# Performance work log

Hardware: AMD Instinct MI355X
Metric: run time of the kernel (lower is better)

Reference implementation:

```python
import jax, jax.numpy as jnp
import numpy as np

B, N, D, H = 4, 2048, 256, 4
HD = D // H


def _linear(x, W, b):
    return x @ W.T + b


def _rotate_half(x):
    # pairs (x0,x1) -> (-x1, x0)
    x1 = x[..., ::2]
    x2 = x[..., 1::2]
    return jnp.stack((-x2, x1), axis=-1).reshape(x.shape)


def _layernorm(x, g, b, eps=1e-5):
    m = jnp.mean(x, axis=-1, keepdims=True)
    v = jnp.mean((x - m) ** 2, axis=-1, keepdims=True)
    return (x - m) / jnp.sqrt(v + eps) * g + b


def _ffn(x, W1, b1, g, be, W2, b2):
    h = _linear(x, W1, b1)
    h = _layernorm(h, g, be)
    h = jax.nn.gelu(h, approximate=False)
    return _linear(h, W2, b2)


def _self_block(x, enc, Wqkv, bqkv, Wout, bout, W1, b1, g, be, W2, b2):
    Bq, Nq, _ = x.shape
    qkv = _linear(x, Wqkv, bqkv).reshape(Bq, Nq, H, HD, 3).transpose(0, 2, 1, 3, 4)  # [B,H,N,HD,3]
    q, k, v = qkv[..., 0], qkv[..., 1], qkv[..., 2]
    q = q * enc[0] + _rotate_half(q) * enc[1]
    k = k * enc[0] + _rotate_half(k) * enc[1]
    scale = HD ** -0.5
    sim = jnp.einsum('bhid,bhjd->bhij', q, k) * scale
    attn = jax.nn.softmax(sim, axis=-1)
    ctx = jnp.einsum('bhij,bhjd->bhid', attn, v)
    msg = _linear(ctx.transpose(0, 2, 1, 3).reshape(Bq, Nq, D), Wout, bout)
    return x + _ffn(jnp.concatenate([x, msg], axis=-1), W1, b1, g, be, W2, b2)


def _cross_block(x0, x1, Wqk, bqk, Wv, bv, Wo, bo, W1, b1, g, be, W2, b2):
    def heads(t):
        return t.reshape(t.shape[0], t.shape[1], H, HD).transpose(0, 2, 1, 3)  # [B,H,N,HD]
    qk0 = heads(_linear(x0, Wqk, bqk))
    qk1 = heads(_linear(x1, Wqk, bqk))
    v0 = heads(_linear(x0, Wv, bv))
    v1 = heads(_linear(x1, Wv, bv))
    s = (HD ** -0.5) ** 0.5
    qk0 = qk0 * s
    qk1 = qk1 * s
    sim = jnp.einsum('bhid,bhjd->bhij', qk0, qk1)
    attn01 = jax.nn.softmax(sim, axis=-1)   # over j (x1 tokens)
    attn10 = jax.nn.softmax(sim, axis=-2)   # over i (x0 tokens)
    m0 = jnp.einsum('bhij,bhjd->bhid', attn01, v1)
    m1 = jnp.einsum('bhij,bhid->bhjd', attn10, v0)
    def unheads(t):
        return t.transpose(0, 2, 1, 3).reshape(t.shape[0], t.shape[2], D)
    m0 = _linear(unheads(m0), Wo, bo)
    m1 = _linear(unheads(m1), Wo, bo)
    x0 = x0 + _ffn(jnp.concatenate([x0, m0], axis=-1), W1, b1, g, be, W2, b2)
    x1 = x1 + _ffn(jnp.concatenate([x1, m1], axis=-1), W1, b1, g, be, W2, b2)
    return x0, x1


def setup_inputs() -> dict:
    key = jax.random.key(0)
    ks = jax.random.split(key, 32)
    std = 0.05

    def rn(k, shape, s=std):
        return jax.random.normal(k, shape, dtype=jnp.float32) * s

    def enc(k):
        ang = jax.random.uniform(k, (B, 1, N, HD // 2), dtype=jnp.float32) * (2 * np.pi)
        cos = jnp.repeat(jnp.cos(ang), 2, axis=-1)
        sin = jnp.repeat(jnp.sin(ang), 2, axis=-1)
        return jnp.stack([cos, sin], axis=0)  # [2,B,1,N,HD]

    return {
        'desc0': rn(ks[0], (B, N, D), 1.0),
        'desc1': rn(ks[1], (B, N, D), 1.0),
        'enc0': enc(ks[2]),
        'enc1': enc(ks[3]),
        's_Wqkv': rn(ks[4], (3 * D, D)), 's_bqkv': jnp.zeros((3 * D,), jnp.float32),
        's_Wout': rn(ks[5], (D, D)), 's_bout': jnp.zeros((D,), jnp.float32),
        's_W1': rn(ks[6], (2 * D, 2 * D)), 's_b1': jnp.zeros((2 * D,), jnp.float32),
        's_g': jnp.ones((2 * D,), jnp.float32), 's_be': jnp.zeros((2 * D,), jnp.float32),
        's_W2': rn(ks[7], (D, 2 * D)), 's_b2': jnp.zeros((D,), jnp.float32),
        'c_Wqk': rn(ks[8], (D, D)), 'c_bqk': jnp.zeros((D,), jnp.float32),
        'c_Wv': rn(ks[9], (D, D)), 'c_bv': jnp.zeros((D,), jnp.float32),
        'c_Wo': rn(ks[10], (D, D)), 'c_bo': jnp.zeros((D,), jnp.float32),
        'c_W1': rn(ks[11], (2 * D, 2 * D)), 'c_b1': jnp.zeros((2 * D,), jnp.float32),
        'c_g': jnp.ones((2 * D,), jnp.float32), 'c_be': jnp.zeros((2 * D,), jnp.float32),
        'c_W2': rn(ks[12], (D, 2 * D)), 'c_b2': jnp.zeros((D,), jnp.float32),
    }


def reference(desc0, desc1, enc0, enc1,
              s_Wqkv, s_bqkv, s_Wout, s_bout, s_W1, s_b1, s_g, s_be, s_W2, s_b2,
              c_Wqk, c_bqk, c_Wv, c_bv, c_Wo, c_bo, c_W1, c_b1, c_g, c_be, c_W2, c_b2):
    d0 = _self_block(desc0, enc0, s_Wqkv, s_bqkv, s_Wout, s_bout, s_W1, s_b1, s_g, s_be, s_W2, s_b2)
    d1 = _self_block(desc1, enc1, s_Wqkv, s_bqkv, s_Wout, s_bout, s_W1, s_b1, s_g, s_be, s_W2, s_b2)
    return _cross_block(d0, d1, c_Wqk, c_bqk, c_Wv, c_bv, c_Wo, c_bo, c_W1, c_b1, c_g, c_be, c_W2, c_b2)
```

## Files before the change

### kernel.cpp

```cpp
#include <hip/hip_runtime.h>
#include <cstddef>

#define NTOK 2048
#define BDIM 4
#define DIM 256
#define NHEAD 4
#define MROWS 8192
#define M2 16384
#define NMu ((size_t)MROWS * DIM)

typedef unsigned short u16;
typedef __attribute__((ext_vector_type(8))) short short8;
typedef __attribute__((ext_vector_type(4))) float f32x4;

#if __has_builtin(__builtin_amdgcn_exp2f)
#define EXP2(x) __builtin_amdgcn_exp2f(x)
#else
#define EXP2(x) exp2f(x)
#endif

__device__ __forceinline__ u16 f2bf(float x) {
  union { float f; unsigned u; } c; c.f = x;
  unsigned r = c.u + 0x7FFFu + ((c.u >> 16) & 1u);
  return (u16)(r >> 16);
}
__device__ __forceinline__ float bf2f(u16 u) {
  union { unsigned u; float f; } c; c.u = ((unsigned)u) << 16;
  return c.f;
}

__device__ __forceinline__ void glds16(const void* g, void* l) {
  __builtin_amdgcn_global_load_lds(
      (const __attribute__((address_space(1))) unsigned int*)g,
      (__attribute__((address_space(3))) unsigned int*)l, 16, 0, 0);
}

__global__ __launch_bounds__(256) void gemm_bf16_kernel(
    const u16* __restrict__ A, int lda,
    const u16* __restrict__ A2, int lda2, int kSplit,
    const u16* __restrict__ W,
    const float* __restrict__ bias0, const float* __restrict__ bias1,
    int nsplit, float os0, float os1,
    u16* __restrict__ Yb0, int ldy0,
    u16* __restrict__ Yb1, int ldy1,
    int K)
{
  __shared__ u16 As[2 * 4096];
  __shared__ u16 Bs[2 * 4096];
  const int t = threadIdx.x;
  const int m0 = blockIdx.y * 128, n0 = blockIdx.x * 128;
  const int r4 = t >> 2, c8 = (t & 3) * 8;
  const int lane = t & 63, w = t >> 6;
  const int cl = lane & 15, quad = lane >> 4;
  const int wm = (w >> 1) * 64, wn = (w & 1) * 64;

  f32x4 acc[4][4];
#pragma unroll
  for (int i = 0; i < 4; ++i)
#pragma unroll
    for (int j = 0; j < 4; ++j) acc[i][j] = (f32x4){0.f, 0.f, 0.f, 0.f};

  for (int k0 = 0; k0 < K; k0 += 64) {
    const u16* Ab; int la; int kk;
    if (k0 < kSplit) { Ab = A; la = lda; kk = k0; }
    else             { Ab = A2; la = lda2; kk = k0 - kSplit; }
    const u16* ag = Ab + (size_t)(m0 + r4) * la + kk + c8;
    const u16* bg = W + (size_t)(n0 + r4) * K + k0 + c8;
    __syncthreads();
#pragma unroll
    for (int kh = 0; kh < 2; ++kh) {
      glds16(ag + kh * 32, &As[kh * 4096 + t * 8]);
      glds16(ag + (size_t)64 * la + kh * 32, &As[kh * 4096 + 2048 + t * 8]);
      glds16(bg + kh * 32, &Bs[kh * 4096 + t * 8]);
      glds16(bg + (size_t)64 * K + kh * 32, &Bs[kh * 4096 + 2048 + t * 8]);
    }
    __syncthreads();

#pragma unroll
    for (int kh = 0; kh < 2; ++kh) {
      short8 af[4], bfr[4];
#pragma unroll
      for (int i = 0; i < 4; ++i)
        af[i] = *(const short8*)&As[kh * 4096 + (wm + i * 16 + cl) * 32 + quad * 8];
#pragma unroll
      for (int i = 0; i < 4; ++i)
        bfr[i] = *(const short8*)&Bs[kh * 4096 + (wn + i * 16 + cl) * 32 + quad * 8];
#pragma unroll
      for (int mt = 0; mt < 4; ++mt)
#pragma unroll
        for (int nt = 0; nt < 4; ++nt)
          acc[mt][nt] = __builtin_amdgcn_mfma_f32_16x16x32_bf16(
              af[mt], bfr[nt], acc[mt][nt], 0, 0, 0);
    }
  }

#pragma unroll
  for (int mt = 0; mt < 4; ++mt)
#pragma unroll
    for (int nt = 0; nt < 4; ++nt) {
      const int colg = n0 + wn + nt * 16 + cl;
      const bool first = colg < nsplit;
      const int c2 = first ? colg : colg - nsplit;
      const float bs = first ? bias0[c2] : bias1[c2];
      const float os = first ? os0 : os1;
      u16* yb = first ? Yb0 : Yb1;
      const int ly = first ? ldy0 : ldy1;
#pragma unroll
      for (int r = 0; r < 4; ++r) {
        const int rowg = m0 + wm + mt * 16 + quad * 4 + r;
        yb[(size_t)rowg * ly + c2] = f2bf((acc[mt][nt][r] + bs) * os);
      }
    }
}

__global__ __launch_bounds__(256) void gemm64_kernel(
    const u16* __restrict__ A, int lda,
    const u16* __restrict__ W,
    const float* __restrict__ bias,
    const u16* __restrict__ resb, int ldrb,
    float* __restrict__ Yf, int ldyf,
    u16* __restrict__ Yb, int ldyb,
    int K)
{
  __shared__ u16 As[2 * 2048];
  __shared__ u16 Bs[2 * 2048];
  const int t = threadIdx.x;
  const int m0 = blockIdx.y * 64, n0 = blockIdx.x * 64;
  const int r8 = t >> 2, c8 = (t & 3) * 8;
  const int lane = t & 63, w = t >> 6;
  const int cl = lane & 15, quad = lane >> 4;
  const int wm = (w >> 1) * 32, wn = (w & 1) * 32;

  f32x4 acc[2][2];
#pragma unroll
  for (int i = 0; i < 2; ++i)
#pragma unroll
    for (int j = 0; j < 2; ++j) acc[i][j] = (f32x4){0.f, 0.f, 0.f, 0.f};

  for (int k0 = 0; k0 < K; k0 += 64) {
    const u16* ag = A + (size_t)(m0 + r8) * lda + k0 + c8;
    const u16* bg = W + (size_t)(n0 + r8) * K + k0 + c8;
    __syncthreads();
#pragma unroll
    for (int kh = 0; kh < 2; ++kh) {
      glds16(ag + kh * 32, &As[kh * 2048 + t * 8]);
      glds16(bg + kh * 32, &Bs[kh * 2048 + t * 8]);
    }
    __syncthreads();

#pragma unroll
    for (int kh = 0; kh < 2; ++kh) {
      short8 af[2], bfr[2];
#pragma unroll
      for (int i = 0; i < 2; ++i)
        af[i] = *(const short8*)&As[kh * 2048 + (wm + i * 16 + cl) * 32 + quad * 8];
#pragma unroll
      for (int j = 0; j < 2; ++j)
        bfr[j] = *(const short8*)&Bs[kh * 2048 + (wn + j * 16 + cl) * 32 + quad * 8];
#pragma unroll
      for (int mt = 0; mt < 2; ++mt)
#pragma unroll
        for (int nt = 0; nt < 2; ++nt)
          acc[mt][nt] = __builtin_amdgcn_mfma_f32_16x16x32_bf16(
              af[mt], bfr[nt], acc[mt][nt], 0, 0, 0);
    }
  }

#pragma unroll
  for (int mt = 0; mt < 2; ++mt)
#pragma unroll
    for (int nt = 0; nt < 2; ++nt) {
      const int colg = n0 + wn + nt * 16 + cl;
      const float bs = bias[colg];
#pragma unroll
      for (int r = 0; r < 4; ++r) {
        const int rowg = m0 + wm + mt * 16 + quad * 4 + r;
        float v = acc[mt][nt][r] + bs;
        if (resb) v += bf2f(resb[(size_t)rowg * ldrb + colg]);
        if (Yf) Yf[(size_t)rowg * ldyf + colg] = v;
        if (Yb) Yb[(size_t)rowg * ldyb + colg] = f2bf(v);
      }
    }
}

__global__ __launch_bounds__(256) void pack_wfuse_kernel(
    const float* w0, const float* w1, const float* w2, const float* w3,
    const float* w4, const float* d0, const float* d1,
    u16* __restrict__ wb, u16* __restrict__ descb,
    const float* __restrict__ W1, const float* __restrict__ Wo,
    const float* __restrict__ b1, const float* __restrict__ bo,
    const float* __restrict__ cW1, const float* __restrict__ cWo,
    const float* __restrict__ cb1, const float* __restrict__ cbo,
    u16* __restrict__ W1f, u16* __restrict__ cW1f,
    float* __restrict__ b1f, float* __restrict__ cb1f)
{
  __shared__ float rowh[256];
  const int bid = blockIdx.x;
  const int t = threadIdx.x;
  if (bid < 4672) {
    const size_t idx4 = ((size_t)bid * 256 + t) * 4;
    const float* src; u16* dst; size_t off;
    if (idx4 < 589824) {
      off = idx4; dst = wb + idx4;
      if      (idx4 < 196608) { src = w0; }
      else if (idx4 < 327680) { src = w1; off -= 196608; }
      else if (idx4 < 393216) { src = w2; off -= 327680; }
      else if (idx4 < 458752) { src = w3; off -= 393216; }
      else                    { src = w4; off -= 458752; }
    } else {
      size_t o = idx4 - 589824;
      dst = descb + o;
      if (o < NMu) { src = d0; off = o; }
      else         { src = d1; off = o - NMu; }
    }
    float4 v = *(const float4*)(src + off);
    ushort4 ov;
    ov.x = f2bf(v.x); ov.y = f2bf(v.y); ov.z = f2bf(v.z); ov.w = f2bf(v.w);
    *(ushort4*)dst = ov;
  } else {
    const int idx = bid - 4672;
    const int n = idx & 511, sel = idx >> 9;
    const float* Ws = sel ? cW1 : W1;
    const float* Wos = sel ? cWo : Wo;
    u16* out = sel ? cW1f : W1f;
    rowh[t] = Ws[(size_t)n * 512 + 256 + t];
    out[(size_t)n * 512 + t] = f2bf(Ws[(size_t)n * 512 + t]);
    __syncthreads();
    float acc = 0.f;
    for (int m = 0; m < 256; ++m) acc += rowh[m] * Wos[(size_t)m * 256 + t];
    out[(size_t)n * 512 + 256 + t] = f2bf(acc);
    if (t == 0) {
      const float* bos = sel ? cbo : bo;
      const float* b1s = sel ? cb1 : b1;
      float a = b1s[n];
      for (int m = 0; m < 256; ++m) a += rowh[m] * bos[m];
      (sel ? cb1f : b1f)[n] = a;
    }
  }
}

__global__ __launch_bounds__(256) void rope_tv_kernel(
    const u16* __restrict__ qkv, const float* __restrict__ enc0,
    const float* __restrict__ enc1,
    u16* __restrict__ Q, u16* __restrict__ K, u16* __restrict__ Vt)
{
  __shared__ u16 Vl[64 * 264];
  const int blk = blockIdx.x;
  const int t = threadIdx.x;
  const int hf = blk >> 7;
  const float* enc = hf ? enc1 : enc0;
  const float QSC = 0.18033688011112042f;

  for (int p = 0; p < 32; ++p) {
    const int j = p * 256 + t;
    const int i = j & 31;
    const int h = (j >> 5) & 3;
    const int lt = j >> 7;
    const int m = blk * 64 + lt;
    const int lm = m & (MROWS - 1);
    const u16* src = qkv + (size_t)m * 768 + h * 192 + i * 6;
    const unsigned a0 = *(const unsigned*)(src);
    const unsigned a1 = *(const unsigned*)(src + 2);
    const unsigned a2 = *(const unsigned*)(src + 4);
    const float q0 = bf2f((u16)a0), k0 = bf2f((u16)(a0 >> 16));
    const float v0 = bf2f((u16)a1), q1 = bf2f((u16)(a1 >> 16));
    const float k1 = bf2f((u16)a2), v1 = bf2f((u16)(a2 >> 16));
    const float c = enc[(size_t)lm * 64 + 2 * i];
    const float s = enc[(size_t)MROWS * 64 + (size_t)lm * 64 + 2 * i];
    const size_t o = (size_t)m * 256 + h * 64 + 2 * i;
    *(unsigned*)(Q + o) = (unsigned)f2bf((q0 * c - q1 * s) * QSC) |
                          ((unsigned)f2bf((q1 * c + q0 * s) * QSC) << 16);
    *(unsigned*)(K + o) = (unsigned)f2bf(k0 * c - k1 * s) |
                          ((unsigned)f2bf(k1 * c + k0 * s) << 16);
    *(unsigned*)&Vl[lt * 264 + h * 64 + 2 * i] =
        (unsigned)f2bf(v0) | ((unsigned)f2bf(v1) << 16);
  }
  __syncthreads();

  const int bz = blk >> 5, n0 = (blk & 31) * 64;
  const int dd = t >> 2, qr = t & 3;
#pragma unroll
  for (int h = 0; h < 4; ++h) {
    union { u16 u[16]; uint4 v[2]; } pk;
#pragma unroll
    for (int jj = 0; jj < 16; ++jj)
      pk.u[jj] = Vl[(qr * 16 + jj) * 264 + h * 64 + dd];
    u16* dst = Vt + ((size_t)((bz * NHEAD + h) * 64 + dd)) * NTOK + n0 + qr * 16;
    *(uint4*)dst = pk.v[0];
    *(uint4*)(dst + 8) = pk.v[1];
  }
}

__global__ __launch_bounds__(256) void transpose_v_kernel(
    const u16* __restrict__ in, u16* __restrict__ out)
{
  __shared__ u16 Tl[64][72];
  const int bz = blockIdx.z, h = blockIdx.y;
  const int n0 = blockIdx.x * 64;
  const int t = threadIdx.x;
  {
    const int row = t >> 2, c16 = (t & 3) * 16;
    const u16* src = in + (size_t)(bz * NTOK + n0 + row) * 256 + h * 64 + c16;
    *(uint4*)&Tl[row][c16] = *(const uint4*)src;
    *(uint4*)&Tl[row][c16 + 8] = *(const uint4*)(src + 8);
  }
  __syncthreads();
  const int d = t >> 2, qr = t & 3;
  union { u16 u[16]; uint4 v[2]; } pk;
#pragma unroll
  for (int j = 0; j < 16; ++j) pk.u[j] = Tl[qr * 16 + j][d];
  u16* dst = out + ((size_t)((bz * NHEAD + h) * 64 + d)) * NTOK + n0 + qr * 16;
  *(uint4*)dst = pk.v[0];
  *(uint4*)(dst + 8) = pk.v[1];
}

__global__ __launch_bounds__(256, 2) void attn5_kernel(
    const u16* __restrict__ Qb, const u16* __restrict__ Kb,
    const u16* __restrict__ Vtb, u16* __restrict__ Ou, int cross)
{
  __shared__ u16 Ks[2][64 * 64];
  __shared__ u16 Vs[2][64 * 64];
  __shared__ u16 Ps[4][32 * 64];

  const int hw = blockIdx.x;
  const int li = hw >> 3;
  const int y  = (hw & 7) * 4 + (li >> 4);
  const int n0 = (li & 15) * 128;

  const int h2 = y >> 4, b = (y >> 2) & 3, h = y & 3;
  const int kh = cross ? (1 - h2) : h2;
  const int qrowbase = (h2 * 4 + b) * NTOK;
  const int krowbase = (kh * 4 + b) * NTOK;
  const int vz = kh * 4 + b;
  const int t = threadIdx.x, lane = t & 63, w = t >> 6;
  const int cl = lane & 15, quad = lane >> 4;
  const int q0 = w * 32;
  const int fsw = (cl & 7) << 4;

  short8 bq[2][2];
#pragma unroll
  for (int c = 0; c < 2; ++c) {
    const u16* qsrc = Qb + (size_t)(qrowbase + n0 + q0 + c * 16 + cl) * 256 +
                      h * 64 + quad * 8;
    bq[c][0] = *(const short8*)qsrc;
    bq[c][1] = *(const short8*)(qsrc + 32);
  }

  float l_r[2] = {0.f, 0.f};
  f32x4 o[2][4];
#pragma unroll
  for (int c = 0; c < 2; ++c)
#pragma unroll
    for (int i = 0; i < 4; ++i) o[c][i] = (f32x4){0.f, 0.f, 0.f, 0.f};

  const int srow = t >> 2;
  const int scb = (t & 3) * 32;
  const int ssw = (srow & 7) << 4;
  const u16* Kg = Kb + (size_t)(krowbase + srow) * 256 + h * 64 + (t & 3) * 16;
  const u16* Vg = Vtb + ((size_t)(vz * NHEAD + h) * 64 + srow) * NTOK + (t & 3) * 16;

  uint4 ka0 = *(const uint4*)Kg, ka1 = *(const uint4*)(Kg + 8);
  uint4 va0 = *(const uint4*)Vg, va1 = *(const uint4*)(Vg + 8);
  {
    char* kd = (char*)&Ks[0][srow * 64];
    *(uint4*)(kd + (scb ^ ssw)) = ka0;
    *(uint4*)(kd + ((scb + 16) ^ ssw)) = ka1;
    char* vd = (char*)&Vs[0][srow * 64];
    *(uint4*)(vd + (scb ^ ssw)) = va0;
    *(uint4*)(vd + ((scb + 16) ^ ssw)) = va1;
  }
  Kg += 64 * 256; Vg += 64;
  ka0 = *(const uint4*)Kg; ka1 = *(const uint4*)(Kg + 8);
  va0 = *(const uint4*)Vg; va1 = *(const uint4*)(Vg + 8);
  __syncthreads();

  for (int tile = 0; tile < 32; ++tile) {
    const int cur = tile & 1, nxt = cur ^ 1;

    f32x4 sf[2][4];
    __builtin_amdgcn_s_setprio(1);
#pragma unroll
    for (int kb = 0; kb < 4; ++kb) {
      const char* kr = (const char*)&Ks[cur][(kb * 16 + cl) * 64];
      short8 ak0 = *(const short8*)(kr + ((quad * 16) ^ fsw));
      short8 ak1 = *(const short8*)(kr + ((quad * 16 + 64) ^ fsw));
#pragma unroll
      for (int c = 0; c < 2; ++c) {
        f32x4 acc = (f32x4){0.f, 0.f, 0.f, 0.f};
        acc = __builtin_amdgcn_mfma_f32_16x16x32_bf16(ak0, bq[c][0], acc, 0, 0, 0);
        acc = __builtin_amdgcn_mfma_f32_16x16x32_bf16(ak1, bq[c][1], acc, 0, 0, 0);
        sf[c][kb] = acc;
      }
    }
    __builtin_amdgcn_s_setprio(0);

    if (tile < 31) {
      char* kd = (char*)&Ks[nxt][srow * 64];
      *(uint4*)(kd + (scb ^ ssw)) = ka0;
      *(uint4*)(kd + ((scb + 16) ^ ssw)) = ka1;
      if (tile < 30) {
        Kg += 64 * 256;
        ka0 = *(const uint4*)Kg; ka1 = *(const uint4*)(Kg + 8);
      }
    }

#pragma unroll
    for (int c = 0; c < 2; ++c) {
      float rs = 0.f;
#pragma unroll
      for (int kb = 0; kb < 4; ++kb)
#pragma unroll
        for (int r = 0; r < 4; ++r) {
          const float p = EXP2(sf[c][kb][r]);
          sf[c][kb][r] = p; rs += p;
        }
      rs += __shfl_xor(rs, 16);
      rs += __shfl_xor(rs, 32);
      l_r[c] += rs;
      char* pd = (char*)&Ps[w][(c * 16 + cl) * 64];
#pragma unroll
      for (int kb = 0; kb < 4; ++kb) {
        unsigned d0 = __builtin_amdgcn_perm(__float_as_uint(sf[c][kb][1]),
                                            __float_as_uint(sf[c][kb][0]), 0x07060302u);
        unsigned d1 = __builtin_amdgcn_perm(__float_as_uint(sf[c][kb][3]),
                                            __float_as_uint(sf[c][kb][2]), 0x07060302u);
        uint2 pk; pk.x = d0; pk.y = d1;
        *(uint2*)(pd + ((kb * 32 + quad * 8) ^ fsw)) = pk;
      }
    }

    short8 bp[2][2];
#pragma unroll
    for (int c = 0; c < 2; ++c) {
      const char* pr = (const char*)&Ps[w][(c * 16 + cl) * 64];
      bp[c][0] = *(const short8*)(pr + ((quad * 16) ^ fsw));
      bp[c][1] = *(const short8*)(pr + ((quad * 16 + 64) ^ fsw));
    }
    __builtin_amdgcn_s_setprio(1);
#pragma unroll
    for (int db = 0; db < 4; ++db) {
      const char* vr = (const char*)&Vs[cur][(db * 16 + cl) * 64];
      short8 av0 = *(const short8*)(vr + ((quad * 16) ^ fsw));
      short8 av1 = *(const short8*)(vr + ((quad * 16 + 64) ^ fsw));
#pragma unroll
      for (int c = 0; c < 2; ++c) {
        o[c][db] = __builtin_amdgcn_mfma_f32_16x16x32_bf16(av0, bp[c][0], o[c][db], 0, 0, 0);
        o[c][db] = __builtin_amdgcn_mfma_f32_16x16x32_bf16(av1, bp[c][1], o[c][db], 0, 0, 0);
      }
    }
    __builtin_amdgcn_s_setprio(0);

    if (tile < 31) {
      char* vd = (char*)&Vs[nxt][srow * 64];
      *(uint4*)(vd + (scb ^ ssw)) = va0;
      *(uint4*)(vd + ((scb + 16) ^ ssw)) = va1;
      if (tile < 30) {
        Vg += 64;
        va0 = *(const uint4*)Vg; va1 = *(const uint4*)(Vg + 8);
      }
    }
    __syncthreads();
  }

#pragma unroll
  for (int c = 0; c < 2; ++c) {
    const float inv = 1.f / l_r[c];
    const size_t rowo = (size_t)(qrowbase + n0 + q0 + c * 16 + cl) * 256 + h * 64;
#pragma unroll
    for (int db = 0; db < 4; ++db) {
      ushort4 st;
      st.x = f2bf(o[c][db][0] * inv); st.y = f2bf(o[c][db][1] * inv);
      st.z = f2bf(o[c][db][2] * inv); st.w = f2bf(o[c][db][3] * inv);
      *(ushort4*)(Ou + rowo + db * 16 + quad * 4) = st;
    }
  }
}

__global__ __launch_bounds__(256) void ln_gelu_kernel(
    const u16* __restrict__ Hm, const float* __restrict__ g,
    const float* __restrict__ be, u16* __restrict__ out)
{
  const int rowi = blockIdx.x * 4 + (threadIdx.x >> 6);
  const int lane = threadIdx.x & 63;
  const u16* row = Hm + (size_t)rowi * 512 + lane * 8;
  u16* orow = out + (size_t)rowi * 512 + lane * 8;
  uint4 raw = *(const uint4*)row;
  float x[8];
  const unsigned* rw = (const unsigned*)&raw;
#pragma unroll
  for (int i = 0; i < 4; ++i) {
    x[2 * i]     = bf2f((u16)rw[i]);
    x[2 * i + 1] = bf2f((u16)(rw[i] >> 16));
  }
  float s = 0.f;
#pragma unroll
  for (int i = 0; i < 8; ++i) s += x[i];
#pragma unroll
  for (int off = 32; off; off >>= 1) s += __shfl_xor(s, off);
  const float mean = s * (1.f / 512.f);
  float s2 = 0.f;
#pragma unroll
  for (int i = 0; i < 8; ++i) { const float d = x[i] - mean; s2 += d * d; }
#pragma unroll
  for (int off = 32; off; off >>= 1) s2 += __shfl_xor(s2, off);
  const float rstd = rsqrtf(s2 * (1.f / 512.f) + 1e-5f);
  unsigned ov[4];
#pragma unroll
  for (int i = 0; i < 4; ++i) {
    const int c = lane * 8 + 2 * i;
    const float y0 = (x[2 * i] - mean) * rstd * g[c] + be[c];
    const float y1 = (x[2 * i + 1] - mean) * rstd * g[c + 1] + be[c + 1];
    const float g0 = 0.5f * y0 * (1.f + erff(y0 * 0.70710678118654752f));
    const float g1 = 0.5f * y1 * (1.f + erff(y1 * 0.70710678118654752f));
    ov[i] = (unsigned)f2bf(g0) | ((unsigned)f2bf(g1) << 16);
  }
  *(uint4*)orow = *(uint4*)ov;
}

extern "C" void kernel_launch(void* const* d_in, const int* in_sizes, int n_in,
                              void* d_out, int out_size, void* d_ws, size_t ws_size,
                              hipStream_t stream) {
  const float* desc0  = (const float*)d_in[0];
  const float* desc1  = (const float*)d_in[1];
  const float* enc0   = (const float*)d_in[2];
  const float* enc1   = (const float*)d_in[3];
  const float* s_Wqkv = (const float*)d_in[4];
  const float* s_bqkv = (const float*)d_in[5];
  const float* s_Wout = (const float*)d_in[6];
  const float* s_bout = (const float*)d_in[7];
  const float* s_W1   = (const float*)d_in[8];
  const float* s_b1   = (const float*)d_in[9];
  const float* s_g    = (const float*)d_in[10];
  const float* s_be   = (const float*)d_in[11];
  const float* s_W2   = (const float*)d_in[12];
  const float* s_b2   = (const float*)d_in[13];
  const float* c_Wqk  = (const float*)d_in[14];
  const float* c_bqk  = (const float*)d_in[15];
  const float* c_Wv   = (const float*)d_in[16];
  const float* c_bv   = (const float*)d_in[17];
  const float* c_Wo   = (const float*)d_in[18];
  const float* c_bo   = (const float*)d_in[19];
  const float* c_W1   = (const float*)d_in[20];
  const float* c_b1   = (const float*)d_in[21];
  const float* c_g    = (const float*)d_in[22];
  const float* c_be   = (const float*)d_in[23];
  const float* c_W2   = (const float*)d_in[24];
  const float* c_b2   = (const float*)d_in[25];

  u16* U = (u16*)d_ws;
  u16* descb = U + 0 * NMu;
  u16* qkvb  = U + 2 * NMu;
  u16* ctxb  = U + 2 * NMu;
  u16* Qu    = U + 8 * NMu;
  u16* Ku    = U + 10 * NMu;
  u16* Vt    = U + 14 * NMu;
  u16* hbufb = U + 12 * NMu;
  u16* hb2   = U + 16 * NMu;
  float* b1f = (float*)(U + 20 * NMu);
  float* cb1f = b1f + 512;
  u16* s_b   = U + 21 * NMu;
  u16* wb    = U + 23 * NMu;

  u16* Wqkvb = wb;
  u16* W2b   = wb + 196608;
  u16* cQKVb = wb + 327680;
  u16* cW2b  = wb + 458752;
  u16* W1f   = wb + 589824;
  u16* cW1f  = wb + 851968;

  float* outf = (float*)d_out;

  const dim3 tv_grid(NTOK / 64, NHEAD, 8);
  const int lng_blocks  = M2 / 4;
  const float csc = 0.42466090014400953f;

  hipLaunchKernelGGL(pack_wfuse_kernel, dim3(5696), dim3(256), 0, stream,
                     s_Wqkv, s_W2, c_Wqk, c_Wv, c_W2, desc0, desc1, wb, descb,
                     s_W1, s_Wout, s_b1, s_bout, c_W1, c_Wo, c_b1, c_bo,
                     W1f, cW1f, b1f, cb1f);

  hipLaunchKernelGGL(gemm_bf16_kernel, dim3(6, 128), dim3(256), 0, stream,
                     descb, 256, (const u16*)nullptr, 0, 1 << 30, Wqkvb,
                     s_bqkv, (const float*)nullptr, 1 << 30, 1.f, 1.f,
                     qkvb, 768, (u16*)nullptr, 0, 256);
  hipLaunchKernelGGL(rope_tv_kernel, dim3(256), dim3(256), 0, stream,
                     qkvb, enc0, enc1, Qu, Ku, Vt);
  hipLaunchKernelGGL(attn5_kernel, dim3(512), dim3(256), 0, stream,
                     Qu, Ku, Vt, ctxb, 0);
  hipLaunchKernelGGL(gemm_bf16_kernel, dim3(4, 128), dim3(256), 0, stream,
                     descb, 256, ctxb, 256, 256, W1f,
                     b1f, (const float*)nullptr, 1 << 30, 1.f, 1.f,
                     hbufb, 512, (u16*)nullptr, 0, 512);
  hipLaunchKernelGGL(ln_gelu_kernel, dim3(lng_blocks), dim3(256), 0, stream,
                     hbufb, s_g, s_be, hb2);
  hipLaunchKernelGGL(gemm64_kernel, dim3(4, 256), dim3(256), 0, stream,
                     hb2, 512, W2b, s_b2, descb, 256,
                     (float*)nullptr, 0, s_b, 256, 512);

  u16* qkb = Qu;
  u16* vb  = Ku;
  hipLaunchKernelGGL(gemm_bf16_kernel, dim3(4, 128), dim3(256), 0, stream,
                     s_b, 256, (const u16*)nullptr, 0, 1 << 30, cQKVb,
                     c_bqk, c_bv, 256, csc, 1.f,
                     qkb, 256, vb, 256, 256);
  hipLaunchKernelGGL(transpose_v_kernel, tv_grid, dim3(256), 0, stream, vb, Vt);
  hipLaunchKernelGGL(attn5_kernel, dim3(512), dim3(256), 0, stream,
                     qkb, qkb, Vt, ctxb, 1);
  hipLaunchKernelGGL(gemm_bf16_kernel, dim3(4, 128), dim3(256), 0, stream,
                     s_b, 256, ctxb, 256, 256, cW1f,
                     cb1f, (const float*)nullptr, 1 << 30, 1.f, 1.f,
                     hbufb, 512, (u16*)nullptr, 0, 512);
  hipLaunchKernelGGL(ln_gelu_kernel, dim3(lng_blocks), dim3(256), 0, stream,
                     hbufb, c_g, c_be, hb2);
  hipLaunchKernelGGL(gemm64_kernel, dim3(4, 256), dim3(256), 0, stream,
                     hb2, 512, cW2b, c_b2, s_b, 256,
                     outf, 256, (u16*)nullptr, 0, 512);
}
```

Baseline: 377.2 us.

## Switch attention to 32x32x16 MFMA and pass P through registers instead of LDS

Rewrites the attention kernel to use 32x32x16 bf16 MFMA tiles in place of 16x16x32 tiles. The QK^T accumulator layout now lines up with the PV operand layout, so the exp'd probabilities are packed with v_cvt_pk_bf16_f32. Half-wave lane swaps then form the A operand, which removes the per-warp LDS write/read of P and its shared buffer. The aim is fewer LDS round trips and fewer MFMA issues per tile. In exchange, the epilogue now writes scalar bf16 stores and shuffles the row sums, which is less coalesced.

```diff
diff --git a/kernel.cpp b/kernel.cpp
--- a/kernel.cpp
+++ b/kernel.cpp
@@ -12,6 +12,7 @@
 typedef unsigned short u16;
 typedef __attribute__((ext_vector_type(8))) short short8;
 typedef __attribute__((ext_vector_type(4))) float f32x4;
+typedef __attribute__((ext_vector_type(16))) float f32x16;
 
 #if __has_builtin(__builtin_amdgcn_exp2f)
 #define EXP2(x) __builtin_amdgcn_exp2f(x)
@@ -27,6 +28,11 @@
 __device__ __forceinline__ float bf2f(u16 u) {
   union { unsigned u; float f; } c; c.u = ((unsigned)u) << 16;
   return c.f;
+}
+__device__ __forceinline__ unsigned cvtpk(float lo, float hi) {
+  unsigned r;
+  asm("v_cvt_pk_bf16_f32 %0, %1, %2" : "=v"(r) : "v"(lo), "v"(hi));
+  return r;
 }
 
 __device__ __forceinline__ void glds16(const void* g, void* l) {
@@ -314,13 +320,12 @@
   *(uint4*)(dst + 8) = pk.v[1];
 }
 
-__global__ __launch_bounds__(256, 2) void attn5_kernel(
+__global__ __launch_bounds__(256, 2) void attn9_kernel(
     const u16* __restrict__ Qb, const u16* __restrict__ Kb,
     const u16* __restrict__ Vtb, u16* __restrict__ Ou, int cross)
 {
   __shared__ u16 Ks[2][64 * 64];
   __shared__ u16 Vs[2][64 * 64];
-  __shared__ u16 Ps[4][32 * 64];
 
   const int hw = blockIdx.x;
   const int li = hw >> 3;
@@ -333,25 +338,22 @@
   const int krowbase = (kh * 4 + b) * NTOK;
   const int vz = kh * 4 + b;
   const int t = threadIdx.x, lane = t & 63, w = t >> 6;
-  const int cl = lane & 15, quad = lane >> 4;
+  const int l31 = lane & 31, hi = lane >> 5;
   const int q0 = w * 32;
-  const int fsw = (cl & 7) << 4;
-
-  short8 bq[2][2];
-#pragma unroll
-  for (int c = 0; c < 2; ++c) {
-    const u16* qsrc = Qb + (size_t)(qrowbase + n0 + q0 + c * 16 + cl) * 256 +
-                      h * 64 + quad * 8;
-    bq[c][0] = *(const short8*)qsrc;
-    bq[c][1] = *(const short8*)(qsrc + 32);
-  }
-
-  float l_r[2] = {0.f, 0.f};
-  f32x4 o[2][4];
-#pragma unroll
-  for (int c = 0; c < 2; ++c)
-#pragma unroll
-    for (int i = 0; i < 4; ++i) o[c][i] = (f32x4){0.f, 0.f, 0.f, 0.f};
+  const int fsw = (l31 & 7) << 4;
+
+  short8 bq[4];
+  {
+    const u16* qsrc = Qb + (size_t)(qrowbase + n0 + q0 + l31) * 256 +
+                      h * 64 + hi * 8;
+#pragma unroll
+    for (int ks = 0; ks < 4; ++ks) bq[ks] = *(const short8*)(qsrc + ks * 16);
+  }
+
+  float l_r = 0.f;
+  f32x16 o0, o1;
+#pragma unroll
+  for (int i = 0; i < 16; ++i) { o0[i] = 0.f; o1[i] = 0.f; }
 
   const int srow = t >> 2;
   const int scb = (t & 3) * 32;
@@ -377,20 +379,17 @@
   for (int tile = 0; tile < 32; ++tile) {
     const int cur = tile & 1, nxt = cur ^ 1;
 
-    f32x4 sf[2][4];
+    f32x16 s0, s1;
+#pragma unroll
+    for (int i = 0; i < 16; ++i) { s0[i] = 0.f; s1[i] = 0.f; }
     __builtin_amdgcn_s_setprio(1);
 #pragma unroll
-    for (int kb = 0; kb < 4; ++kb) {
-      const char* kr = (const char*)&Ks[cur][(kb * 16 + cl) * 64];
-      short8 ak0 = *(const short8*)(kr + ((quad * 16) ^ fsw));
-      short8 ak1 = *(const short8*)(kr + ((quad * 16 + 64) ^ fsw));
-#pragma unroll
-      for (int c = 0; c < 2; ++c) {
-        f32x4 acc = (f32x4){0.f, 0.f, 0.f, 0.f};
-        acc = __builtin_amdgcn_mfma_f32_16x16x32_bf16(ak0, bq[c][0], acc, 0, 0, 0);
-        acc = __builtin_amdgcn_mfma_f32_16x16x32_bf16(ak1, bq[c][1], acc, 0, 0, 0);
-        sf[c][kb] = acc;
-      }
+    for (int ks = 0; ks < 4; ++ks) {
+      const int ofs = (ks * 32 + hi * 16) ^ fsw;
+      short8 ak0 = *(const short8*)((const char*)&Ks[cur][l31 * 64] + ofs);
+      short8 ak1 = *(const short8*)((const char*)&Ks[cur][(32 + l31) * 64] + ofs);
+      s0 = __builtin_amdgcn_mfma_f32_32x32x16_bf16(ak0, bq[ks], s0, 0, 0, 0);
+      s1 = __builtin_amdgcn_mfma_f32_32x32x16_bf16(ak1, bq[ks], s1, 0, 0, 0);
     }
     __builtin_amdgcn_s_setprio(0);
 
@@ -404,51 +403,42 @@
       }
     }
 
-#pragma unroll
-    for (int c = 0; c < 2; ++c) {
-      float rs = 0.f;
-#pragma unroll
-      for (int kb = 0; kb < 4; ++kb)
-#pragma unroll
-        for (int r = 0; r < 4; ++r) {
-          const float p = EXP2(sf[c][kb][r]);
-          sf[c][kb][r] = p; rs += p;
-        }
-      rs += __shfl_xor(rs, 16);
-      rs += __shfl_xor(rs, 32);
-      l_r[c] += rs;
-      char* pd = (char*)&Ps[w][(c * 16 + cl) * 64];
-#pragma unroll
-      for (int kb = 0; kb < 4; ++kb) {
-        unsigned d0 = __builtin_amdgcn_perm(__float_as_uint(sf[c][kb][1]),
-                                            __float_as_uint(sf[c][kb][0]), 0x07060302u);
-        unsigned d1 = __builtin_amdgcn_perm(__float_as_uint(sf[c][kb][3]),
-                                            __float_as_uint(sf[c][kb][2]), 0x07060302u);
-        uint2 pk; pk.x = d0; pk.y = d1;
-        *(uint2*)(pd + ((kb * 32 + quad * 8) ^ fsw)) = pk;
+    float rs = 0.f;
+#pragma unroll
+    for (int kg = 0; kg < 2; ++kg) {
+      float p[16];
+#pragma unroll
+      for (int r = 0; r < 16; ++r) {
+        p[r] = EXP2(kg ? s1[r] : s0[r]);
+        rs += p[r];
       }
-    }
-
-    short8 bp[2][2];
-#pragma unroll
-    for (int c = 0; c < 2; ++c) {
-      const char* pr = (const char*)&Ps[w][(c * 16 + cl) * 64];
-      bp[c][0] = *(const short8*)(pr + ((quad * 16) ^ fsw));
-      bp[c][1] = *(const short8*)(pr + ((quad * 16 + 64) ^ fsw));
-    }
-    __builtin_amdgcn_s_setprio(1);
-#pragma unroll
-    for (int db = 0; db < 4; ++db) {
-      const char* vr = (const char*)&Vs[cur][(db * 16 + cl) * 64];
-      short8 av0 = *(const short8*)(vr + ((quad * 16) ^ fsw));
-      short8 av1 = *(const short8*)(vr + ((quad * 16 + 64) ^ fsw));
-#pragma unroll
-      for (int c = 0; c < 2; ++c) {
-        o[c][db] = __builtin_amdgcn_mfma_f32_16x16x32_bf16(av0, bp[c][0], o[c][db], 0, 0, 0);
-        o[c][db] = __builtin_amdgcn_mfma_f32_16x16x32_bf16(av1, bp[c][1], o[c][db], 0, 0, 0);
+      unsigned pa4[4], pb4[4], xa4[4], xb4[4];
+#pragma unroll
+      for (int g = 0; g < 4; ++g) {
+        pa4[g] = cvtpk(p[4 * g], p[4 * g + 1]);
+        pb4[g] = cvtpk(p[4 * g + 2], p[4 * g + 3]);
+        xa4[g] = (unsigned)__shfl_xor((int)pa4[g], 32);
+        xb4[g] = (unsigned)__shfl_xor((int)pb4[g], 32);
       }
-    }
-    __builtin_amdgcn_s_setprio(0);
+      __builtin_amdgcn_s_setprio(1);
+#pragma unroll
+      for (int k2 = 0; k2 < 2; ++k2) {
+        const int g0 = (2 * k2) & 3, g1 = (2 * k2 + 1) & 3;
+        union { unsigned u[4]; short8 s; } pa;
+        pa.u[0] = hi ? xa4[g1] : pa4[g0];
+        pa.u[1] = hi ? xb4[g1] : pb4[g0];
+        pa.u[2] = hi ? pa4[g1] : xa4[g0];
+        pa.u[3] = hi ? pb4[g1] : xb4[g0];
+        const int ks = kg * 2 + k2;
+        const int ofs = (ks * 32 + hi * 16) ^ fsw;
+        short8 bv0 = *(const short8*)((const char*)&Vs[cur][l31 * 64] + ofs);
+        short8 bv1 = *(const short8*)((const char*)&Vs[cur][(32 + l31) * 64] + ofs);
+        o0 = __builtin_amdgcn_mfma_f32_32x32x16_bf16(pa.s, bv0, o0, 0, 0, 0);
+        o1 = __builtin_amdgcn_mfma_f32_32x32x16_bf16(pa.s, bv1, o1, 0, 0, 0);
+      }
+      __builtin_amdgcn_s_setprio(0);
+    }
+    l_r += rs + __shfl_xor(rs, 32);
 
     if (tile < 31) {
       char* vd = (char*)&Vs[nxt][srow * 64];
@@ -463,16 +453,13 @@
   }
 
 #pragma unroll
-  for (int c = 0; c < 2; ++c) {
-    const float inv = 1.f / l_r[c];
-    const size_t rowo = (size_t)(qrowbase + n0 + q0 + c * 16 + cl) * 256 + h * 64;
-#pragma unroll
-    for (int db = 0; db < 4; ++db) {
-      ushort4 st;
-      st.x = f2bf(o[c][db][0] * inv); st.y = f2bf(o[c][db][1] * inv);
-      st.z = f2bf(o[c][db][2] * inv); st.w = f2bf(o[c][db][3] * inv);
-      *(ushort4*)(Ou + rowo + db * 16 + quad * 4) = st;
-    }
+  for (int r = 0; r < 16; ++r) {
+    const int qrow = (r & 3) + 8 * (r >> 2) + 4 * hi;
+    const float lq = __shfl(l_r, qrow);
+    const float inv = 1.f / lq;
+    const size_t rowo = (size_t)(qrowbase + n0 + q0 + qrow) * 256 + h * 64;
+    Ou[rowo + l31]      = f2bf(o0[r] * inv);
+    Ou[rowo + 32 + l31] = f2bf(o1[r] * inv);
   }
 }
 
@@ -585,7 +572,7 @@
                      qkvb, 768, (u16*)nullptr, 0, 256);
   hipLaunchKernelGGL(rope_tv_kernel, dim3(256), dim3(256), 0, stream,
                      qkvb, enc0, enc1, Qu, Ku, Vt);
-  hipLaunchKernelGGL(attn5_kernel, dim3(512), dim3(256), 0, stream,
+  hipLaunchKernelGGL(attn9_kernel, dim3(512), dim3(256), 0, stream,
                      Qu, Ku, Vt, ctxb, 0);
   hipLaunchKernelGGL(gemm_bf16_kernel, dim3(4, 128), dim3(256), 0, stream,
                      descb, 256, ctxb, 256, 256, W1f,
@@ -604,7 +591,7 @@
                      c_bqk, c_bv, 256, csc, 1.f,
                      qkb, 256, vb, 256, 256);
   hipLaunchKernelGGL(transpose_v_kernel, tv_grid, dim3(256), 0, stream, vb, Vt);
-  hipLaunchKernelGGL(attn5_kernel, dim3(512), dim3(256), 0, stream,
+  hipLaunchKernelGGL(attn9_kernel, dim3(512), dim3(256), 0, stream,
                      qkb, qkb, Vt, ctxb, 1);
   hipLaunchKernelGGL(gemm_bf16_kernel, dim3(4, 128), dim3(256), 0, stream,
                      s_b, 256, ctxb, 256, 256, cW1f,
```

Result: no change. 384.6 us (+2.0%).

## Prefetch next GEMM K-tile into registers while computing current tile

Applied to the files above, without the earlier changes.

Both bf16 GEMM kernels drop direct global-to-LDS loads and instead stage the next K tile in registers. Those loads are issued before the MFMA work on the current tile and written to LDS after it. The aim is to hide global memory latency behind compute without needing a second LDS buffer. The cost is extra VGPRs for the staging registers, possible occupancy loss, and explicit LDS writes replacing the async LDS loads.

```diff
diff --git a/kernel.cpp b/kernel.cpp
--- a/kernel.cpp
+++ b/kernel.cpp
@@ -29,11 +29,34 @@
   return c.f;
 }
 
-__device__ __forceinline__ void glds16(const void* g, void* l) {
-  __builtin_amdgcn_global_load_lds(
-      (const __attribute__((address_space(1))) unsigned int*)g,
-      (__attribute__((address_space(3))) unsigned int*)l, 16, 0, 0);
-}
+#define GB_GLOAD(k0)                                                       \
+  {                                                                        \
+    const u16* Ab; int la; int kk;                                         \
+    if ((k0) < kSplit) { Ab = A;  la = lda;  kk = (k0); }                  \
+    else               { Ab = A2; la = lda2; kk = (k0) - kSplit; }         \
+    const u16* ag = Ab + (size_t)(m0 + r4) * la + kk + c8;                 \
+    const u16* bg = W + (size_t)(n0 + r4) * K + (k0) + c8;                 \
+    ra[0] = *(const uint4*)(ag);                                           \
+    ra[1] = *(const uint4*)(ag + (size_t)64 * la);                         \
+    ra[2] = *(const uint4*)(ag + 32);                                      \
+    ra[3] = *(const uint4*)(ag + (size_t)64 * la + 32);                    \
+    rb[0] = *(const uint4*)(bg);                                           \
+    rb[1] = *(const uint4*)(bg + (size_t)64 * K);                          \
+    rb[2] = *(const uint4*)(bg + 32);                                      \
+    rb[3] = *(const uint4*)(bg + (size_t)64 * K + 32);                     \
+  }
+
+#define GB_LWRITE()                                                        \
+  {                                                                        \
+    *(uint4*)&As[t * 8]               = ra[0];                             \
+    *(uint4*)&As[2048 + t * 8]        = ra[1];                             \
+    *(uint4*)&As[4096 + t * 8]        = ra[2];                             \
+    *(uint4*)&As[4096 + 2048 + t * 8] = ra[3];                             \
+    *(uint4*)&Bs[t * 8]               = rb[0];                             \
+    *(uint4*)&Bs[2048 + t * 8]        = rb[1];                             \
+    *(uint4*)&Bs[4096 + t * 8]        = rb[2];                             \
+    *(uint4*)&Bs[4096 + 2048 + t * 8] = rb[3];                             \
+  }
 
 __global__ __launch_bounds__(256) void gemm_bf16_kernel(
     const u16* __restrict__ A, int lda,
@@ -60,21 +83,14 @@
 #pragma unroll
     for (int j = 0; j < 4; ++j) acc[i][j] = (f32x4){0.f, 0.f, 0.f, 0.f};
 
+  uint4 ra[4], rb[4];
+  GB_GLOAD(0);
+  GB_LWRITE();
+  __syncthreads();
+
   for (int k0 = 0; k0 < K; k0 += 64) {
-    const u16* Ab; int la; int kk;
-    if (k0 < kSplit) { Ab = A; la = lda; kk = k0; }
-    else             { Ab = A2; la = lda2; kk = k0 - kSplit; }
-    const u16* ag = Ab + (size_t)(m0 + r4) * la + kk + c8;
-    const u16* bg = W + (size_t)(n0 + r4) * K + k0 + c8;
-    __syncthreads();
-#pragma unroll
-    for (int kh = 0; kh < 2; ++kh) {
-      glds16(ag + kh * 32, &As[kh * 4096 + t * 8]);
-      glds16(ag + (size_t)64 * la + kh * 32, &As[kh * 4096 + 2048 + t * 8]);
-      glds16(bg + kh * 32, &Bs[kh * 4096 + t * 8]);
-      glds16(bg + (size_t)64 * K + kh * 32, &Bs[kh * 4096 + 2048 + t * 8]);
-    }
-    __syncthreads();
+    const bool more = (k0 + 64 < K);
+    if (more) GB_GLOAD(k0 + 64);
 
 #pragma unroll
     for (int kh = 0; kh < 2; ++kh) {
@@ -91,6 +107,12 @@
         for (int nt = 0; nt < 4; ++nt)
           acc[mt][nt] = __builtin_amdgcn_mfma_f32_16x16x32_bf16(
               af[mt], bfr[nt], acc[mt][nt], 0, 0, 0);
+    }
+
+    if (more) {
+      __syncthreads();
+      GB_LWRITE();
+      __syncthreads();
     }
   }
 
@@ -137,16 +159,31 @@
 #pragma unroll
     for (int j = 0; j < 2; ++j) acc[i][j] = (f32x4){0.f, 0.f, 0.f, 0.f};
 
+  uint4 ra[2], rb[2];
+#define G64_GLOAD(k0)                                                      \
+  {                                                                        \
+    const u16* ag = A + (size_t)(m0 + r8) * lda + (k0) + c8;               \
+    const u16* bg = W + (size_t)(n0 + r8) * K + (k0) + c8;                 \
+    ra[0] = *(const uint4*)(ag);                                           \
+    ra[1] = *(const uint4*)(ag + 32);                                      \
+    rb[0] = *(const uint4*)(bg);                                           \
+    rb[1] = *(const uint4*)(bg + 32);                                      \
+  }
+#define G64_LWRITE()                                                       \
+  {                                                                        \
+    *(uint4*)&As[t * 8]        = ra[0];                                    \
+    *(uint4*)&As[2048 + t * 8] = ra[1];                                    \
+    *(uint4*)&Bs[t * 8]        = rb[0];                                    \
+    *(uint4*)&Bs[2048 + t * 8] = rb[1];                                    \
+  }
+
+  G64_GLOAD(0);
+  G64_LWRITE();
+  __syncthreads();
+
   for (int k0 = 0; k0 < K; k0 += 64) {
-    const u16* ag = A + (size_t)(m0 + r8) * lda + k0 + c8;
-    const u16* bg = W + (size_t)(n0 + r8) * K + k0 + c8;
-    __syncthreads();
-#pragma unroll
-    for (int kh = 0; kh < 2; ++kh) {
-      glds16(ag + kh * 32, &As[kh * 2048 + t * 8]);
-      glds16(bg + kh * 32, &Bs[kh * 2048 + t * 8]);
-    }
-    __syncthreads();
+    const bool more = (k0 + 64 < K);
+    if (more) G64_GLOAD(k0 + 64);
 
 #pragma unroll
     for (int kh = 0; kh < 2; ++kh) {
@@ -163,6 +200,12 @@
         for (int nt = 0; nt < 2; ++nt)
           acc[mt][nt] = __builtin_amdgcn_mfma_f32_16x16x32_bf16(
               af[mt], bfr[nt], acc[mt][nt], 0, 0, 0);
+    }
+
+    if (more) {
+      __syncthreads();
+      G64_LWRITE();
+      __syncthreads();
     }
   }
 
```

Result: slower. 525.5 us (+39.3%).
